# Optimization experiments

Measured on AMD Instinct MI355X. Metric: run time of the kernel, lower is better.

Reference implementation:

```python
import jax, jax.numpy as jnp
import numpy as np

NUM_RBF = 16
RBF_D_MIN, RBF_D_MAX = 2.0, 22.0
CB_A, CB_B, CB_C = -0.58273431, 0.56802827, -0.54067466
TOP_K = 32
MAX_REL = 32
NPOS = 16
HID = 128
LN_EPS = 1e-5


def _gather_nodes(nodes, idx):
    # nodes: (B, L, D), idx: (B, L, K) -> (B, L, K, D)
    return jax.vmap(lambda n, i: n[i])(nodes, idx)


def _rbf_encode(D):
    mu = jnp.linspace(RBF_D_MIN, RBF_D_MAX, NUM_RBF, dtype=D.dtype)
    sigma = (RBF_D_MAX - RBF_D_MIN) / NUM_RBF
    return jnp.exp(-((D[..., None] - mu) ** 2) / (sigma ** 2))


def setup_inputs() -> dict:
    key = jax.random.key(0)
    ks = jax.random.split(key, 4)
    B, L = 2, 2048
    X = jax.random.normal(ks[0], (B, L, 4, 3), jnp.float32) * 10.0
    residue_mask = jnp.ones((B, L), jnp.float32)
    R_idx = jnp.arange(B * L, dtype=jnp.int32).reshape(B, L)
    chain_labels = jnp.zeros((B, L), jnp.int32)
    # learned params
    W_pos = jax.random.normal(ks[1], (NPOS, 2 * MAX_REL + 2), jnp.float32) * 0.05
    b_pos = jnp.zeros((NPOS,), jnp.float32)
    W_edge = jax.random.normal(ks[2], (HID, 25 * NUM_RBF + NPOS), jnp.float32) * 0.02
    ln_gamma = jnp.ones((HID,), jnp.float32)
    ln_beta = jnp.zeros((HID,), jnp.float32)
    return {"X": X, "residue_mask": residue_mask, "R_idx": R_idx,
            "chain_labels": chain_labels, "W_pos": W_pos, "b_pos": b_pos,
            "W_edge": W_edge, "ln_gamma": ln_gamma, "ln_beta": ln_beta}


def reference(X, residue_mask, R_idx, chain_labels, W_pos, b_pos, W_edge, ln_gamma, ln_beta):
    B, L = X.shape[0], X.shape[1]
    K = min(TOP_K, L)
    # virtual CB from backbone N, CA, C
    N, CA, C = X[..., 0, :], X[..., 1, :], X[..., 2, :]
    b = CA - N
    c = C - CA
    a = jnp.cross(b, c, axis=-1)
    CB = (CB_A * a + CB_B * b + CB_C * c + CA)[..., None, :]
    atoms_5 = jnp.concatenate([X, CB], axis=-2)  # (B, L, 5, 3)
    # kNN on CA coords with invalid residues pushed far away
    diff = CA[:, :, None, :] - CA[:, None, :, :]
    dist_sq = jnp.sum(diff * diff, axis=-1)  # (B, L, L)
    inv_mask = 1.0 - residue_mask
    dist_sq = dist_sq + inv_mask[:, None, :] * 1e6
    _, E_idx = jax.lax.top_k(-dist_sq, K)  # smallest-k indices, (B, L, K)
    # gather neighbor 5-atom coords and compute 25 pairwise distances
    Xf = atoms_5.reshape(B, L, 15)
    Xg = _gather_nodes(Xf, E_idx).reshape(B, L, K, 5, 3)
    d2 = jnp.sum((atoms_5[:, :, None, :, None, :] - Xg[:, :, :, None, :, :]) ** 2, axis=-1)
    D = jnp.sqrt(d2 + 1e-6)  # (B, L, K, 5, 5)
    rbf = _rbf_encode(D).reshape(B, L, K, 25 * NUM_RBF)
    # positional encodings (standard ProteinMPNN form)
    Rg = _gather_nodes(R_idx[..., None], E_idx)[..., 0]  # (B, L, K)
    Cg = _gather_nodes(chain_labels[..., None], E_idx)[..., 0]
    d_rel = Rg - R_idx[:, :, None]
    same_chain = (Cg == chain_labels[:, :, None])
    d_clip = jnp.clip(d_rel + MAX_REL, 0, 2 * MAX_REL)
    d_final = jnp.where(same_chain, d_clip, 2 * MAX_REL + 1)
    oh = jax.nn.one_hot(d_final, 2 * MAX_REL + 2, dtype=rbf.dtype)
    pos_enc = jnp.einsum('blkc,pc->blkp', oh, W_pos) + b_pos
    # edge embedding + layernorm
    edge_input = jnp.concatenate([pos_enc, rbf], axis=-1)  # (B, L, K, 416)
    h = jnp.einsum('blkf,hf->blkh', edge_input, W_edge)
    mean = jnp.mean(h, axis=-1, keepdims=True)
    var = jnp.var(h, axis=-1, keepdims=True)
    E = (h - mean) * jax.lax.rsqrt(var + LN_EPS) * ln_gamma + ln_beta
    return E_idx, E
```

## Files before the change

kernel.cpp:

```cpp
#include <hip/hip_runtime.h>
#include <hip/hip_bf16.h>

#define LEN   2048
#define KNB   32
#define HID   128
#define FS    440
#define FBSZ  (32 * FS)

typedef unsigned long long ull;
typedef unsigned int uint32;
typedef float f32x4  __attribute__((ext_vector_type(4)));
typedef float f32x16 __attribute__((ext_vector_type(16)));

__device__ __forceinline__ void bar_lgkm() {
    asm volatile("s_waitcnt lgkmcnt(0)" ::: "memory");
    __builtin_amdgcn_s_barrier();
    asm volatile("" ::: "memory");
}

__global__ __launch_bounds__(256) void topk_kernel(
    const float* __restrict__ X, const float* __restrict__ mask,
    const float* __restrict__ W_edge, int* __restrict__ Wf8,
    float* __restrict__ eidx_out) {
    const int bid = blockIdx.x;
    const int tid = threadIdx.x;

    if (bid >= 2 * LEN) {
        const int t = (bid - 2 * LEN) * 256 + tid;
        if (t < 13312) {
            const float4 w = ((const float4*)W_edge)[t];
            int r = __builtin_amdgcn_cvt_pk_fp8_f32(w.x, w.y, 0, false);
            r = __builtin_amdgcn_cvt_pk_fp8_f32(w.z, w.w, r, true);
            Wf8[t] = r;
        }
        return;
    }

    const int row = bid;
    const int b = row >> 11;
    const int i = row & (LEN - 1);

    __shared__ int hist[512];
    __shared__ ull cand[LEN];
    __shared__ int candcnt;
    __shared__ int selB;

    const float* Xb = X + (size_t)b * LEN * 12;
    const float* mb = mask + (size_t)b * LEN;
    const float cax = Xb[i * 12 + 3];
    const float cay = Xb[i * 12 + 4];
    const float caz = Xb[i * 12 + 5];

    uint32 d2b[8];
#pragma unroll
    for (int q = 0; q < 8; ++q) {
        const int j = q * 256 + tid;
        float dx = __fsub_rn(cax, Xb[j * 12 + 3]);
        float dy = __fsub_rn(cay, Xb[j * 12 + 4]);
        float dz = __fsub_rn(caz, Xb[j * 12 + 5]);
        float d2 = __fadd_rn(__fadd_rn(__fmul_rn(dx, dx), __fmul_rn(dy, dy)),
                             __fmul_rn(dz, dz));
        d2 = __fadd_rn(d2, __fmul_rn(__fsub_rn(1.0f, mb[j]), 1000000.0f));
        d2b[q] = __float_as_uint(d2);
    }

    hist[tid] = 0; hist[tid + 256] = 0;
    if (tid == 0) candcnt = 0;
    __syncthreads();
#pragma unroll
    for (int q = 0; q < 8; ++q) atomicAdd(&hist[d2b[q] >> 22], 1);
    __syncthreads();

    if (tid < 64) {
        int loc[8];
        int s = 0;
#pragma unroll
        for (int t = 0; t < 8; ++t) { loc[t] = hist[tid * 8 + t]; s += loc[t]; }
        int incl = s;
#pragma unroll
        for (int off = 1; off < 64; off <<= 1) {
            int o = __shfl_up(incl, off, 64);
            if (tid >= off) incl += o;
        }
        const int excl = incl - s;
        if (excl < KNB && incl >= KNB) {
            int c = excl;
#pragma unroll
            for (int t = 0; t < 8; ++t) {
                int c2 = c + loc[t];
                if (c < KNB && c2 >= KNB) selB = tid * 8 + t;
                c = c2;
            }
        }
    }
    __syncthreads();
    const uint32 B = (uint32)selB;

#pragma unroll
    for (int q = 0; q < 8; ++q) {
        if ((d2b[q] >> 22) <= B) {
            int p = atomicAdd(&candcnt, 1);
            cand[p] = (((ull)d2b[q]) << 32) | (uint32)(q * 256 + tid);
        }
    }
    __syncthreads();
    const int M = candcnt;

    for (int c = tid; c < M; c += 256) {
        const ull k = cand[c];
        int r = 0;
        for (int m = 0; m < M; ++m) r += (cand[m] < k);
        if (r < KNB)
            eidx_out[(size_t)row * KNB + r] = (float)(uint32)(k & 0xFFFFFFFFull);
    }
}

__device__ __forceinline__ void load_res_atoms(const float* __restrict__ p, float* dst) {
    const float Nx = p[0], Ny = p[1], Nz = p[2];
    const float Ax = p[3], Ay = p[4], Az = p[5];
    const float Cx = p[6], Cy = p[7], Cz = p[8];
    const float Ox = p[9], Oy = p[10], Oz = p[11];
    const float bx = Ax - Nx, by = Ay - Ny, bz = Az - Nz;
    const float cx = Cx - Ax, cy = Cy - Ay, cz = Cz - Az;
    const float axv = by * cz - bz * cy;
    const float ayv = bz * cx - bx * cz;
    const float azv = bx * cy - by * cx;
    dst[0] = Nx;  dst[1] = Ny;  dst[2] = Nz;
    dst[3] = Ax;  dst[4] = Ay;  dst[5] = Az;
    dst[6] = Cx;  dst[7] = Cy;  dst[8] = Cz;
    dst[9] = Ox;  dst[10] = Oy; dst[11] = Oz;
    dst[12] = -0.58273431f * axv + 0.56802827f * bx + -0.54067466f * cx + Ax;
    dst[13] = -0.58273431f * ayv + 0.56802827f * by + -0.54067466f * cy + Ay;
    dst[14] = -0.58273431f * azv + 0.56802827f * bz + -0.54067466f * cz + Az;
}

__device__ __forceinline__ int pk4(float a, float b, float c, float d) {
    int r = __builtin_amdgcn_cvt_pk_fp8_f32(a, b, 0, false);
    return __builtin_amdgcn_cvt_pk_fp8_f32(c, d, r, true);
}

#define E1  3.2053337e-1f
#define E3  3.2931300e-2f
#define E5  3.3834001e-3f
#define E7  3.4760500e-4f

__device__ __forceinline__ void compute_features(
    int tid, int Ri, int Ci,
    const __bf16* __restrict__ wposL,
    const int* jR, const int* jC,
    const float (*natoms)[15], const float* iatoms,
    unsigned char* featF8) {
    {
        const int e = tid >> 4, p = tid & 15;
        const int drel = jR[e] - Ri;
        const int same = (jC[e] == Ci);
        int dc = drel + 32;
        dc = dc < 0 ? 0 : (dc > 64 ? 64 : dc);
        const int df = same ? dc : 65;
        const float v = (float)wposL[p * 66 + df];
        const int pb = __builtin_amdgcn_cvt_pk_fp8_f32(v, 0.0f, 0, false);
        featF8[e * FS + p] = (unsigned char)(pb & 0xFF);
    }
#pragma unroll
    for (int it = 0; it < 2; ++it) {
        const int task = tid + it * 512;
        if (task < 800) {
            const int mn = task >> 5, e = task & 31;
            const int m = mn / 5, n = mn - m * 5;
            const float ax = iatoms[m * 3 + 0];
            const float ay = iatoms[m * 3 + 1];
            const float az = iatoms[m * 3 + 2];
            const float* na = &natoms[e][n * 3];
            const float dx = ax - na[0], dy = ay - na[1], dz = az - na[2];
            const float D = sqrtf(dx * dx + dy * dy + dz * dz + 1e-6f);
            const float Dc = fminf(D, 40.0f);
            const float v4 = Dc - 7.3333333f;
            const float A4  = __expf(-0.64f * v4 * v4);
            const float C4  = __expf(1.7066667f * v4);
            const float Ci4 = 1.0f / C4;
            ull lo, hi2;
            {
                const float f3 = A4 * Ci4 * E1;
                const float f2 = f3 * Ci4 * E3;
                const float f1 = f2 * Ci4 * E5;
                const float f0 = f1 * Ci4 * E7;
                const float f5 = A4 * C4 * E1;
                const float f6 = f5 * C4 * E3;
                const float f7 = f6 * C4 * E5;
                lo = (uint32)pk4(f0, f1, f2, f3)
                   | ((ull)(uint32)pk4(A4, f5, f6, f7) << 32);
            }
            const float v12 = Dc - 18.0f;
            const float A12  = __expf(-0.64f * v12 * v12);
            const float C12  = C4 * 1.24140e-8f;
            const float Ci12 = Ci4 * 8.05543e7f;
            {
                const float f11 = A12 * Ci12 * E1;
                const float f10 = f11 * Ci12 * E3;
                const float f9  = f10 * Ci12 * E5;
                const float f8  = f9  * Ci12 * E7;
                const float f13 = A12 * C12 * E1;
                const float f14 = f13 * C12 * E3;
                const float f15 = f14 * C12 * E5;
                hi2 = (uint32)pk4(f8, f9, f10, f11)
                    | ((ull)(uint32)pk4(A12, f13, f14, f15) << 32);
            }
            *(ull*)(featF8 + e * FS + 16 + mn * 16)     = lo;
            *(ull*)(featF8 + e * FS + 16 + mn * 16 + 8) = hi2;
        }
    }
}

__device__ __forceinline__ f32x16 gemm26(const unsigned char* fb, const long* wreg) {
    f32x16 acc = {0.f, 0.f, 0.f, 0.f, 0.f, 0.f, 0.f, 0.f,
                  0.f, 0.f, 0.f, 0.f, 0.f, 0.f, 0.f, 0.f};
#pragma unroll
    for (int ks = 0; ks < 26; ++ks) {
        const long a = *(const long*)(fb + ks * 16);
        acc = __builtin_amdgcn_mfma_f32_32x32x16_fp8_fp8(wreg[ks], a, acc, 0, 0, 0);
    }
    return acc;
}

__device__ __forceinline__ void partials(
    const f32x16& acc, float (*pSb)[4], float (*pQb)[4],
    int e32, int cg, int hi) {
    float s = 0.f, q = 0.f;
#pragma unroll
    for (int r = 0; r < 16; ++r) { s += acc[r]; q += acc[r] * acc[r]; }
    s += __shfl_xor(s, 32, 64);
    q += __shfl_xor(q, 32, 64);
    if (hi == 0) { pSb[e32][cg] = s; pQb[e32][cg] = q; }
}

__device__ __forceinline__ void ln_store(
    const f32x16& acc, const float (*pSb)[4], const float (*pQb)[4],
    int e32, int cg, int hi, int myrow,
    const float* gbuf, const float* bbuf, float* __restrict__ outE) {
    const float4 ps = *(const float4*)&pSb[e32][0];
    const float4 pq = *(const float4*)&pQb[e32][0];
    const float s = ps.x + ps.y + ps.z + ps.w;
    const float q = pq.x + pq.y + pq.z + pq.w;
    const float mean = s * (1.0f / 128.0f);
    const float rstd = rsqrtf(q * (1.0f / 128.0f) - mean * mean + 1e-5f);
    const int cb = cg * 32 + hi * 4;
    float* orow = outE + ((size_t)myrow * KNB + e32) * HID + cb;
#pragma unroll
    for (int j = 0; j < 4; ++j) {
        const float4 gg = *(const float4*)&gbuf[cb + 8 * j];
        const float4 bb = *(const float4*)&bbuf[cb + 8 * j];
        float4 o;
        o.x = (acc[4 * j + 0] - mean) * rstd * gg.x + bb.x;
        o.y = (acc[4 * j + 1] - mean) * rstd * gg.y + bb.y;
        o.z = (acc[4 * j + 2] - mean) * rstd * gg.z + bb.z;
        o.w = (acc[4 * j + 3] - mean) * rstd * gg.w + bb.w;
        *(float4*)(orow + 8 * j) = o;
    }
}

__global__ __launch_bounds__(512, 4) void edge_kernel(
    const float* __restrict__ X,
    const int* __restrict__ Ridx, const int* __restrict__ Chain,
    const float* __restrict__ W_pos, const float* __restrict__ b_pos,
    const unsigned char* __restrict__ Wf8,
    const float* __restrict__ lng, const float* __restrict__ lnb,
    const float* __restrict__ eidx_f, float* __restrict__ outE) {
    const int tid = threadIdx.x;
    const int row0 = blockIdx.x * 8;
    const int b = row0 >> 11;
    const int i0 = row0 & (LEN - 1);

    __shared__ __align__(16) unsigned char featF8[4 * FBSZ];
    __shared__ float natoms[8][32][15];
    __shared__ float iatoms[8][16];
    __shared__ __bf16 wposL[16 * 66];
    __shared__ __align__(16) float pS[2][2][32][4];
    __shared__ __align__(16) float pQ[2][2][32][4];
    __shared__ float gbuf[HID], bbuf[HID];
    __shared__ int jR[8][KNB], jC[8][KNB];
    __shared__ int riS[8], ciS[8];

    const float* Xb = X + (size_t)b * LEN * 12;

    const int w = tid >> 6, l = tid & 63;
    const int rowsel = w >> 2, cg = w & 3;
    const int e32 = l & 31, hi = l >> 5;

    long wreg[26];
    {
        const unsigned char* wb = Wf8 + (size_t)(cg * 32 + e32) * 416 + hi * 8;
#pragma unroll
        for (int ks = 0; ks < 26; ++ks)
            wreg[ks] = *(const long*)(wb + ks * 16);
    }

    for (int t = tid; t < 1056; t += 512)
        wposL[t] = (__bf16)(W_pos[t] + b_pos[t / 66]);
    if (tid < 256) {
        const int r = tid >> 5, e = tid & 31;
        const int j = (int)eidx_f[(size_t)(row0 + r) * KNB + e];
        jR[r][e] = Ridx[b * LEN + j];
        jC[r][e] = Chain[b * LEN + j];
        load_res_atoms(Xb + j * 12, &natoms[r][e][0]);
    } else if (tid < 264) {
        const int r = tid - 256;
        load_res_atoms(Xb + (size_t)(i0 + r) * 12, &iatoms[r][0]);
    } else if (tid < 272) {
        riS[tid - 264] = Ridx[b * LEN + i0 + (tid - 264)];
    } else if (tid < 280) {
        ciS[tid - 272] = Chain[b * LEN + i0 + (tid - 272)];
    } else if (tid >= 384) {
        const int t2 = tid - 384;
        gbuf[t2] = lng[t2];
        bbuf[t2] = lnb[t2];
    }
    bar_lgkm();

    compute_features(tid, riS[0], ciS[0], wposL, jR[0], jC[0],
                     natoms[0], iatoms[0], featF8 + 0 * FBSZ);
    compute_features(tid, riS[1], ciS[1], wposL, jR[1], jC[1],
                     natoms[1], iatoms[1], featF8 + 1 * FBSZ);
    bar_lgkm();

    const unsigned char* fbMine01 = featF8 + rowsel * FBSZ + e32 * FS + hi * 8;
    const unsigned char* fbMine23 = featF8 + ((2 + rowsel) & 3) * FBSZ + e32 * FS + hi * 8;

    f32x16 accA, accB;

    accA = gemm26(fbMine01, wreg);
    compute_features(tid, riS[2], ciS[2], wposL, jR[2], jC[2],
                     natoms[2], iatoms[2], featF8 + 2 * FBSZ);
    compute_features(tid, riS[3], ciS[3], wposL, jR[3], jC[3],
                     natoms[3], iatoms[3], featF8 + 3 * FBSZ);
    partials(accA, pS[0][rowsel], pQ[0][rowsel], e32, cg, hi);
    bar_lgkm();

    ln_store(accA, pS[0][rowsel], pQ[0][rowsel], e32, cg, hi,
             row0 + 0 + rowsel, gbuf, bbuf, outE);
    accB = gemm26(fbMine23, wreg);
    compute_features(tid, riS[4], ciS[4], wposL, jR[4], jC[4],
                     natoms[4], iatoms[4], featF8 + 0 * FBSZ);
    compute_features(tid, riS[5], ciS[5], wposL, jR[5], jC[5],
                     natoms[5], iatoms[5], featF8 + 1 * FBSZ);
    partials(accB, pS[1][rowsel], pQ[1][rowsel], e32, cg, hi);
    bar_lgkm();

    ln_store(accB, pS[1][rowsel], pQ[1][rowsel], e32, cg, hi,
             row0 + 2 + rowsel, gbuf, bbuf, outE);
    accA = gemm26(fbMine01, wreg);
    compute_features(tid, riS[6], ciS[6], wposL, jR[6], jC[6],
                     natoms[6], iatoms[6], featF8 + 2 * FBSZ);
    compute_features(tid, riS[7], ciS[7], wposL, jR[7], jC[7],
                     natoms[7], iatoms[7], featF8 + 3 * FBSZ);
    partials(accA, pS[0][rowsel], pQ[0][rowsel], e32, cg, hi);
    bar_lgkm();

    ln_store(accA, pS[0][rowsel], pQ[0][rowsel], e32, cg, hi,
             row0 + 4 + rowsel, gbuf, bbuf, outE);
    accB = gemm26(fbMine23, wreg);
    partials(accB, pS[1][rowsel], pQ[1][rowsel], e32, cg, hi);
    bar_lgkm();

    ln_store(accB, pS[1][rowsel], pQ[1][rowsel], e32, cg, hi,
             row0 + 6 + rowsel, gbuf, bbuf, outE);
}

extern "C" void kernel_launch(void* const* d_in, const int* in_sizes, int n_in,
                              void* d_out, int out_size, void* d_ws, size_t ws_size,
                              hipStream_t stream) {
    const float* X      = (const float*)d_in[0];
    const float* mask   = (const float*)d_in[1];
    const int*   Ridx   = (const int*)d_in[2];
    const int*   Chain  = (const int*)d_in[3];
    const float* W_pos  = (const float*)d_in[4];
    const float* b_pos  = (const float*)d_in[5];
    const float* W_edge = (const float*)d_in[6];
    const float* lng    = (const float*)d_in[7];
    const float* lnb    = (const float*)d_in[8];

    float* out  = (float*)d_out;
    float* eidx = out;
    float* E    = out + (size_t)2 * LEN * KNB;

    unsigned char* Wf8 = (unsigned char*)d_ws;

    const int nrow = 2 * LEN;
    topk_kernel<<<nrow + 52, 256, 0, stream>>>(X, mask, W_edge, (int*)Wf8, eidx);
    edge_kernel<<<nrow / 8, 512, 0, stream>>>(X, Ridx, Chain, W_pos, b_pos, Wf8,
                                              lng, lnb, eidx, E);
}
```

Measured before the change: 56.10 us.

## Shrink edge kernel to 256-thread blocks of 4 rows with bf16 atom staging

```diff
diff --git a/kernel.cpp b/kernel.cpp
--- a/kernel.cpp
+++ b/kernel.cpp
@@ -115,7 +115,7 @@
     }
 }
 
-__device__ __forceinline__ void load_res_atoms(const float* __restrict__ p, float* dst) {
+__device__ __forceinline__ void load_res_atoms_bf(const float* __restrict__ p, __bf16* dst) {
     const float Nx = p[0], Ny = p[1], Nz = p[2];
     const float Ax = p[3], Ay = p[4], Az = p[5];
     const float Cx = p[6], Cy = p[7], Cz = p[8];
@@ -125,13 +125,14 @@
     const float axv = by * cz - bz * cy;
     const float ayv = bz * cx - bx * cz;
     const float azv = bx * cy - by * cx;
-    dst[0] = Nx;  dst[1] = Ny;  dst[2] = Nz;
-    dst[3] = Ax;  dst[4] = Ay;  dst[5] = Az;
-    dst[6] = Cx;  dst[7] = Cy;  dst[8] = Cz;
-    dst[9] = Ox;  dst[10] = Oy; dst[11] = Oz;
-    dst[12] = -0.58273431f * axv + 0.56802827f * bx + -0.54067466f * cx + Ax;
-    dst[13] = -0.58273431f * ayv + 0.56802827f * by + -0.54067466f * cy + Ay;
-    dst[14] = -0.58273431f * azv + 0.56802827f * bz + -0.54067466f * cz + Az;
+    dst[0] = (__bf16)Nx;  dst[1] = (__bf16)Ny;  dst[2] = (__bf16)Nz;
+    dst[3] = (__bf16)Ax;  dst[4] = (__bf16)Ay;  dst[5] = (__bf16)Az;
+    dst[6] = (__bf16)Cx;  dst[7] = (__bf16)Cy;  dst[8] = (__bf16)Cz;
+    dst[9] = (__bf16)Ox;  dst[10] = (__bf16)Oy; dst[11] = (__bf16)Oz;
+    dst[12] = (__bf16)(-0.58273431f * axv + 0.56802827f * bx + -0.54067466f * cx + Ax);
+    dst[13] = (__bf16)(-0.58273431f * ayv + 0.56802827f * by + -0.54067466f * cy + Ay);
+    dst[14] = (__bf16)(-0.58273431f * azv + 0.56802827f * bz + -0.54067466f * cz + Az);
+    dst[15] = (__bf16)0.0f;
 }
 
 __device__ __forceinline__ int pk4(float a, float b, float c, float d) {
@@ -148,10 +149,12 @@
     int tid, int Ri, int Ci,
     const __bf16* __restrict__ wposL,
     const int* jR, const int* jC,
-    const float (*natoms)[15], const float* iatoms,
+    const __bf16 (*natoms)[16], const __bf16* iatoms,
     unsigned char* featF8) {
-    {
-        const int e = tid >> 4, p = tid & 15;
+#pragma unroll
+    for (int it = 0; it < 2; ++it) {
+        const int task = tid + it * 256;
+        const int e = task >> 4, p = task & 15;
         const int drel = jR[e] - Ri;
         const int same = (jC[e] == Ci);
         int dc = drel + 32;
@@ -161,53 +164,50 @@
         const int pb = __builtin_amdgcn_cvt_pk_fp8_f32(v, 0.0f, 0, false);
         featF8[e * FS + p] = (unsigned char)(pb & 0xFF);
     }
-#pragma unroll
-    for (int it = 0; it < 2; ++it) {
-        const int task = tid + it * 512;
-        if (task < 800) {
-            const int mn = task >> 5, e = task & 31;
-            const int m = mn / 5, n = mn - m * 5;
-            const float ax = iatoms[m * 3 + 0];
-            const float ay = iatoms[m * 3 + 1];
-            const float az = iatoms[m * 3 + 2];
-            const float* na = &natoms[e][n * 3];
-            const float dx = ax - na[0], dy = ay - na[1], dz = az - na[2];
-            const float D = sqrtf(dx * dx + dy * dy + dz * dz + 1e-6f);
-            const float Dc = fminf(D, 40.0f);
-            const float v4 = Dc - 7.3333333f;
-            const float A4  = __expf(-0.64f * v4 * v4);
-            const float C4  = __expf(1.7066667f * v4);
-            const float Ci4 = 1.0f / C4;
-            ull lo, hi2;
-            {
-                const float f3 = A4 * Ci4 * E1;
-                const float f2 = f3 * Ci4 * E3;
-                const float f1 = f2 * Ci4 * E5;
-                const float f0 = f1 * Ci4 * E7;
-                const float f5 = A4 * C4 * E1;
-                const float f6 = f5 * C4 * E3;
-                const float f7 = f6 * C4 * E5;
-                lo = (uint32)pk4(f0, f1, f2, f3)
-                   | ((ull)(uint32)pk4(A4, f5, f6, f7) << 32);
-            }
-            const float v12 = Dc - 18.0f;
-            const float A12  = __expf(-0.64f * v12 * v12);
-            const float C12  = C4 * 1.24140e-8f;
-            const float Ci12 = Ci4 * 8.05543e7f;
-            {
-                const float f11 = A12 * Ci12 * E1;
-                const float f10 = f11 * Ci12 * E3;
-                const float f9  = f10 * Ci12 * E5;
-                const float f8  = f9  * Ci12 * E7;
-                const float f13 = A12 * C12 * E1;
-                const float f14 = f13 * C12 * E3;
-                const float f15 = f14 * C12 * E5;
-                hi2 = (uint32)pk4(f8, f9, f10, f11)
-                    | ((ull)(uint32)pk4(A12, f13, f14, f15) << 32);
-            }
-            *(ull*)(featF8 + e * FS + 16 + mn * 16)     = lo;
-            *(ull*)(featF8 + e * FS + 16 + mn * 16 + 8) = hi2;
-        }
+    for (int task = tid; task < 800; task += 256) {
+        const int mn = task >> 5, e = task & 31;
+        const int m = mn / 5, n = mn - m * 5;
+        const float ax = (float)iatoms[m * 3 + 0];
+        const float ay = (float)iatoms[m * 3 + 1];
+        const float az = (float)iatoms[m * 3 + 2];
+        const float dx = ax - (float)natoms[e][n * 3 + 0];
+        const float dy = ay - (float)natoms[e][n * 3 + 1];
+        const float dz = az - (float)natoms[e][n * 3 + 2];
+        const float D = sqrtf(dx * dx + dy * dy + dz * dz + 1e-6f);
+        const float Dc = fminf(D, 40.0f);
+        const float v4 = Dc - 7.3333333f;
+        const float A4  = __expf(-0.64f * v4 * v4);
+        const float C4  = __expf(1.7066667f * v4);
+        const float Ci4 = 1.0f / C4;
+        ull lo, hi2;
+        {
+            const float f3 = A4 * Ci4 * E1;
+            const float f2 = f3 * Ci4 * E3;
+            const float f1 = f2 * Ci4 * E5;
+            const float f0 = f1 * Ci4 * E7;
+            const float f5 = A4 * C4 * E1;
+            const float f6 = f5 * C4 * E3;
+            const float f7 = f6 * C4 * E5;
+            lo = (uint32)pk4(f0, f1, f2, f3)
+               | ((ull)(uint32)pk4(A4, f5, f6, f7) << 32);
+        }
+        const float v12 = Dc - 18.0f;
+        const float A12  = __expf(-0.64f * v12 * v12);
+        const float C12  = C4 * 1.24140e-8f;
+        const float Ci12 = Ci4 * 8.05543e7f;
+        {
+            const float f11 = A12 * Ci12 * E1;
+            const float f10 = f11 * Ci12 * E3;
+            const float f9  = f10 * Ci12 * E5;
+            const float f8  = f9  * Ci12 * E7;
+            const float f13 = A12 * C12 * E1;
+            const float f14 = f13 * C12 * E3;
+            const float f15 = f14 * C12 * E5;
+            hi2 = (uint32)pk4(f8, f9, f10, f11)
+                | ((ull)(uint32)pk4(A12, f13, f14, f15) << 32);
+        }
+        *(ull*)(featF8 + e * FS + 16 + mn * 16)     = lo;
+        *(ull*)(featF8 + e * FS + 16 + mn * 16 + 8) = hi2;
     }
 }
 
@@ -258,7 +258,7 @@
     }
 }
 
-__global__ __launch_bounds__(512, 4) void edge_kernel(
+__global__ __launch_bounds__(256, 4) void edge_kernel(
     const float* __restrict__ X,
     const int* __restrict__ Ridx, const int* __restrict__ Chain,
     const float* __restrict__ W_pos, const float* __restrict__ b_pos,
@@ -266,24 +266,22 @@
     const float* __restrict__ lng, const float* __restrict__ lnb,
     const float* __restrict__ eidx_f, float* __restrict__ outE) {
     const int tid = threadIdx.x;
-    const int row0 = blockIdx.x * 8;
+    const int row0 = blockIdx.x * 4;
     const int b = row0 >> 11;
     const int i0 = row0 & (LEN - 1);
 
-    __shared__ __align__(16) unsigned char featF8[4 * FBSZ];
-    __shared__ float natoms[8][32][15];
-    __shared__ float iatoms[8][16];
+    __shared__ __align__(16) unsigned char featF8[2][FBSZ];
+    __shared__ __align__(4) __bf16 natoms[4][32][16];
+    __shared__ __bf16 iatoms[4][16];
     __shared__ __bf16 wposL[16 * 66];
-    __shared__ __align__(16) float pS[2][2][32][4];
-    __shared__ __align__(16) float pQ[2][2][32][4];
+    __shared__ __align__(16) float pS[2][32][4], pQ[2][32][4];
     __shared__ float gbuf[HID], bbuf[HID];
-    __shared__ int jR[8][KNB], jC[8][KNB];
-    __shared__ int riS[8], ciS[8];
+    __shared__ int jR[4][KNB], jC[4][KNB];
+    __shared__ int riS[4], ciS[4];
 
     const float* Xb = X + (size_t)b * LEN * 12;
 
-    const int w = tid >> 6, l = tid & 63;
-    const int rowsel = w >> 2, cg = w & 3;
+    const int cg = tid >> 6, l = tid & 63;
     const int e32 = l & 31, hi = l >> 5;
 
     long wreg[26];
@@ -294,75 +292,60 @@
             wreg[ks] = *(const long*)(wb + ks * 16);
     }
 
-    for (int t = tid; t < 1056; t += 512)
+    for (int t = tid; t < 1056; t += 256)
         wposL[t] = (__bf16)(W_pos[t] + b_pos[t / 66]);
-    if (tid < 256) {
+    if (tid < 128) {
         const int r = tid >> 5, e = tid & 31;
         const int j = (int)eidx_f[(size_t)(row0 + r) * KNB + e];
         jR[r][e] = Ridx[b * LEN + j];
         jC[r][e] = Chain[b * LEN + j];
-        load_res_atoms(Xb + j * 12, &natoms[r][e][0]);
-    } else if (tid < 264) {
-        const int r = tid - 256;
-        load_res_atoms(Xb + (size_t)(i0 + r) * 12, &iatoms[r][0]);
-    } else if (tid < 272) {
-        riS[tid - 264] = Ridx[b * LEN + i0 + (tid - 264)];
-    } else if (tid < 280) {
-        ciS[tid - 272] = Chain[b * LEN + i0 + (tid - 272)];
-    } else if (tid >= 384) {
-        const int t2 = tid - 384;
-        gbuf[t2] = lng[t2];
-        bbuf[t2] = lnb[t2];
+        load_res_atoms_bf(Xb + j * 12, &natoms[r][e][0]);
+        gbuf[tid] = lng[tid];
+        bbuf[tid] = lnb[tid];
+    } else if (tid < 132) {
+        const int r = tid - 128;
+        load_res_atoms_bf(Xb + (size_t)(i0 + r) * 12, &iatoms[r][0]);
+    } else if (tid < 136) {
+        riS[tid - 132] = Ridx[b * LEN + i0 + (tid - 132)];
+    } else if (tid < 140) {
+        ciS[tid - 136] = Chain[b * LEN + i0 + (tid - 136)];
     }
     bar_lgkm();
 
     compute_features(tid, riS[0], ciS[0], wposL, jR[0], jC[0],
-                     natoms[0], iatoms[0], featF8 + 0 * FBSZ);
+                     natoms[0], iatoms[0], featF8[0]);
+    bar_lgkm();
+
+    const unsigned char* fb0 = featF8[0] + e32 * FS + hi * 8;
+    const unsigned char* fb1 = featF8[1] + e32 * FS + hi * 8;
+    f32x16 acc;
+
+    acc = gemm26(fb0, wreg);
     compute_features(tid, riS[1], ciS[1], wposL, jR[1], jC[1],
-                     natoms[1], iatoms[1], featF8 + 1 * FBSZ);
-    bar_lgkm();
-
-    const unsigned char* fbMine01 = featF8 + rowsel * FBSZ + e32 * FS + hi * 8;
-    const unsigned char* fbMine23 = featF8 + ((2 + rowsel) & 3) * FBSZ + e32 * FS + hi * 8;
-
-    f32x16 accA, accB;
-
-    accA = gemm26(fbMine01, wreg);
+                     natoms[1], iatoms[1], featF8[1]);
+    partials(acc, pS[0], pQ[0], e32, cg, hi);
+    bar_lgkm();
+
+    ln_store(acc, pS[0], pQ[0], e32, cg, hi, row0 + 0, gbuf, bbuf, outE);
+    acc = gemm26(fb1, wreg);
     compute_features(tid, riS[2], ciS[2], wposL, jR[2], jC[2],
-                     natoms[2], iatoms[2], featF8 + 2 * FBSZ);
+                     natoms[2], iatoms[2], featF8[0]);
+    partials(acc, pS[1], pQ[1], e32, cg, hi);
+    bar_lgkm();
+
+    ln_store(acc, pS[1], pQ[1], e32, cg, hi, row0 + 1, gbuf, bbuf, outE);
+    acc = gemm26(fb0, wreg);
     compute_features(tid, riS[3], ciS[3], wposL, jR[3], jC[3],
-                     natoms[3], iatoms[3], featF8 + 3 * FBSZ);
-    partials(accA, pS[0][rowsel], pQ[0][rowsel], e32, cg, hi);
-    bar_lgkm();
-
-    ln_store(accA, pS[0][rowsel], pQ[0][rowsel], e32, cg, hi,
-             row0 + 0 + rowsel, gbuf, bbuf, outE);
-    accB = gemm26(fbMine23, wreg);
-    compute_features(tid, riS[4], ciS[4], wposL, jR[4], jC[4],
-                     natoms[4], iatoms[4], featF8 + 0 * FBSZ);
-    compute_features(tid, riS[5], ciS[5], wposL, jR[5], jC[5],
-                     natoms[5], iatoms[5], featF8 + 1 * FBSZ);
-    partials(accB, pS[1][rowsel], pQ[1][rowsel], e32, cg, hi);
-    bar_lgkm();
-
-    ln_store(accB, pS[1][rowsel], pQ[1][rowsel], e32, cg, hi,
-             row0 + 2 + rowsel, gbuf, bbuf, outE);
-    accA = gemm26(fbMine01, wreg);
-    compute_features(tid, riS[6], ciS[6], wposL, jR[6], jC[6],
-                     natoms[6], iatoms[6], featF8 + 2 * FBSZ);
-    compute_features(tid, riS[7], ciS[7], wposL, jR[7], jC[7],
-                     natoms[7], iatoms[7], featF8 + 3 * FBSZ);
-    partials(accA, pS[0][rowsel], pQ[0][rowsel], e32, cg, hi);
-    bar_lgkm();
-
-    ln_store(accA, pS[0][rowsel], pQ[0][rowsel], e32, cg, hi,
-             row0 + 4 + rowsel, gbuf, bbuf, outE);
-    accB = gemm26(fbMine23, wreg);
-    partials(accB, pS[1][rowsel], pQ[1][rowsel], e32, cg, hi);
-    bar_lgkm();
-
-    ln_store(accB, pS[1][rowsel], pQ[1][rowsel], e32, cg, hi,
-             row0 + 6 + rowsel, gbuf, bbuf, outE);
+                     natoms[3], iatoms[3], featF8[1]);
+    partials(acc, pS[0], pQ[0], e32, cg, hi);
+    bar_lgkm();
+
+    ln_store(acc, pS[0], pQ[0], e32, cg, hi, row0 + 2, gbuf, bbuf, outE);
+    acc = gemm26(fb1, wreg);
+    partials(acc, pS[1], pQ[1], e32, cg, hi);
+    bar_lgkm();
+
+    ln_store(acc, pS[1], pQ[1], e32, cg, hi, row0 + 3, gbuf, bbuf, outE);
 }
 
 extern "C" void kernel_launch(void* const* d_in, const int* in_sizes, int n_in,
@@ -386,6 +369,6 @@
 
     const int nrow = 2 * LEN;
     topk_kernel<<<nrow + 52, 256, 0, stream>>>(X, mask, W_edge, (int*)Wf8, eidx);
-    edge_kernel<<<nrow / 8, 512, 0, stream>>>(X, Ridx, Chain, W_pos, b_pos, Wf8,
+    edge_kernel<<<nrow / 4, 256, 0, stream>>>(X, Ridx, Chain, W_pos, b_pos, Wf8,
                                               lng, lnb, eidx, E);
 }
```

New measurement: 54.20 us. 1.04x faster.
